# Performance work log

Measured on AMD Instinct MI355X. Metric: run time of the kernel, lower is better.

## Reference

```python
import jax, jax.numpy as jnp
import numpy as np

BLOCK = 8
C = 64


def setup_inputs() -> dict:
    key = jax.random.key(0)
    k = jax.random.split(key, 6)
    B, H, W = 4, 512, 512
    x = jax.random.normal(k[0], (B, C, H, W), jnp.float32)
    # per-channel 8x8 transform matrices (torch.randn init)
    tw = jax.random.normal(k[1], (C, BLOCK, BLOCK), jnp.float32)
    s = 1.0 / np.sqrt(C).astype(np.float32)
    w1 = jax.random.normal(k[2], (C, C), jnp.float32) * s  # 1x1 conv weight [out,in]
    b1 = jax.random.normal(k[3], (C,), jnp.float32) * s
    w2 = jax.random.normal(k[4], (C, C), jnp.float32) * s
    b2 = jax.random.normal(k[5], (C,), jnp.float32) * s
    return {"x": x, "tw": tw, "w1": w1, "b1": b1, "w2": w2, "b2": b2}


def reference(x, tw, w1, b1, w2, b2):
    B, Cc, H, W = x.shape
    bs = BLOCK
    nh, nw = H // bs, W // bs
    # extract 8x8 blocks: [b,c,nh,nw,i,j]
    p = x.reshape(B, Cc, nh, bs, nw, bs).transpose(0, 1, 2, 4, 3, 5)
    # per-channel T @ P @ T^T : out[p,q] = T[p,i] P[i,j] T[q,j]
    t = jnp.einsum('cpi,bcnmij,cqj->bcnmpq', tw, p, tw)
    # fold blocks back to image
    y = t.transpose(0, 1, 2, 4, 3, 5).reshape(B, Cc, H, W)
    # quantization gate: 1x1 conv -> relu -> 1x1 conv -> sigmoid
    g = jnp.einsum('oc,bchw->bohw', w1, y) + b1[None, :, None, None]
    g = jax.nn.relu(g)
    g = jnp.einsum('oc,bchw->bohw', w2, g) + b2[None, :, None, None]
    g = jax.nn.sigmoid(g)
    return y * g
```

## Files before the change

kernel.cpp:

```cpp
#include <hip/hip_runtime.h>

typedef float f4 __attribute__((ext_vector_type(4)));
typedef __attribute__((ext_vector_type(4))) float f32x4;
typedef _Float16 h8 __attribute__((ext_vector_type(8)));

__device__ __forceinline__ void gload_lds16(const float* g, float* l) {
    __builtin_amdgcn_global_load_lds(
        (const __attribute__((address_space(1))) void*)g,
        (__attribute__((address_space(3))) void*)l, 16, 0, 0);
}

__global__ __launch_bounds__(256, 2)
void avif_pipe2(const float* __restrict__ x, const float* __restrict__ twm,
                const float* __restrict__ w1, const float* __restrict__ b1,
                const float* __restrict__ w2, const float* __restrict__ b2,
                float* __restrict__ out)
{
    __shared__ float xs[8192];
    __shared__ ushort ysf[128][64];
    __shared__ ushort hsf[128][64];

    const int t = threadIdx.x;
    const int bid = blockIdx.x;
    const int wc  = bid >> 8;
    const int rem = bid & 255;
    const int hb  = rem & 63;
    const int b   = rem >> 6;

    const int wv = t >> 6, lane = t & 63;
    const int li = lane & 15, lg = lane >> 4, l7 = li & 7;
    const int lb3 = (li >> 3) << 2;

    const float* xslab = x + (((size_t)(b * 64)) * 512 + (size_t)hb * 8) * 512 + wc * 16;
    const float* gp[8];
#pragma unroll
    for (int j = 0; j < 8; ++j) {
        const int G = j * 256 + t;
        const int c = G >> 5;
        const int v = (G & 31) ^ (c & 7);
        const int r = v >> 2, qg = v & 3;
        gp[j] = xslab + (size_t)c * 262144 + r * 512 + qg * 4;
    }
    float* lbase = &xs[wv * 256];

    h8 w1f[2], w2f[2];
    {
        const float* p1 = w1 + (16 * wv + li) * 64 + lg * 8;
        const float* p2 = w2 + (16 * wv + li) * 64 + lg * 8;
#pragma unroll
        for (int kk = 0; kk < 2; ++kk) {
            f4 a = *(const f4*)(p1 + kk * 32);
            f4 d = *(const f4*)(p1 + kk * 32 + 4);
            h8 f;
#pragma unroll
            for (int q = 0; q < 4; ++q) { f[q] = (_Float16)a[q]; f[4 + q] = (_Float16)d[q]; }
            w1f[kk] = f;
            a = *(const f4*)(p2 + kk * 32);
            d = *(const f4*)(p2 + kk * 32 + 4);
#pragma unroll
            for (int q = 0; q < 4; ++q) { f[q] = (_Float16)a[q]; f[4 + q] = (_Float16)d[q]; }
            w2f[kk] = f;
        }
    }
    const int o0 = 16 * wv + 4 * lg;
    const f4 b1v = *(const f4*)(b1 + o0);
    const float b2s = b2[16 * wv + li];
    const int sg0 = ((lg       ^ l7 ^ lb3) << 3);
    const int sg1 = (((4 + lg) ^ l7 ^ lb3) << 3);
    const int go  = o0 >> 3, co = 4 * (lg & 1);
    const int ch  = 16 * wv + li;
    const int cgE = ch >> 3, c7E = li & 7;

    const int pid = t >> 1, h2 = t & 1;
    const int c   = pid & 63, blk = pid >> 6, Q0 = 4 * h2;
    const float* tB = twm + c * 64;
    const int sc = c * 128, swc = c & 7;
    const int cg = c >> 3, c7 = c & 7;

#pragma unroll
    for (int j = 0; j < 8; ++j) gload_lds16(gp[j], lbase + j * 1024);
    asm volatile("s_waitcnt vmcnt(0)" ::: "memory");
    __syncthreads();

    for (int tile = 0; tile < 16; ++tile) {
        const int wt = 2 * tile + wc;

        {
            float M[8][4];
            {
                f4 Ph[8];
#pragma unroll
                for (int i = 0; i < 8; ++i)
                    Ph[i] = *(const f4*)&xs[sc + ((i * 4 + blk * 2) ^ swc) * 4];
#pragma unroll
                for (int qq = 0; qq < 4; ++qq) {
                    f4 Th = *(const f4*)(tB + (Q0 + qq) * 8);
#pragma unroll
                    for (int i = 0; i < 8; ++i) {
                        float s = Ph[i][0] * Th[0];
                        s = fmaf(Ph[i][1], Th[1], s);
                        s = fmaf(Ph[i][2], Th[2], s);
                        s = fmaf(Ph[i][3], Th[3], s);
                        M[i][qq] = s;
                    }
                }
#pragma unroll
                for (int i = 0; i < 8; ++i)
                    Ph[i] = *(const f4*)&xs[sc + ((i * 4 + blk * 2 + 1) ^ swc) * 4];
#pragma unroll
                for (int qq = 0; qq < 4; ++qq) {
                    f4 Th = *(const f4*)(tB + (Q0 + qq) * 8 + 4);
#pragma unroll
                    for (int i = 0; i < 8; ++i) {
                        float s = M[i][qq];
                        s = fmaf(Ph[i][0], Th[0], s);
                        s = fmaf(Ph[i][1], Th[1], s);
                        s = fmaf(Ph[i][2], Th[2], s);
                        s = fmaf(Ph[i][3], Th[3], s);
                        M[i][qq] = s;
                    }
                }
            }
#pragma unroll
            for (int p = 0; p < 8; ++p) {
                f4 a = *(const f4*)(tB + p * 8);
                f4 d = *(const f4*)(tB + p * 8 + 4);
                const int px0 = p * 16 + blk * 8;
#pragma unroll
                for (int qq = 0; qq < 4; ++qq) {
                    const int q = Q0 + qq;
                    float s = a[0] * M[0][qq];
                    s = fmaf(a[1], M[1][qq], s);
                    s = fmaf(a[2], M[2][qq], s);
                    s = fmaf(a[3], M[3][qq], s);
                    s = fmaf(d[0], M[4][qq], s);
                    s = fmaf(d[1], M[5][qq], s);
                    s = fmaf(d[2], M[6][qq], s);
                    s = fmaf(d[3], M[7][qq], s);
                    const int idx = ((cg ^ q ^ (blk << 2)) << 3) | c7;
                    *(_Float16*)&ysf[px0 + q][idx] = (_Float16)s;
                }
            }
        }
        __syncthreads();

        if (tile < 15) {
#pragma unroll
            for (int j = 0; j < 8; ++j)
                gload_lds16(gp[j] + (tile + 1) * 32, lbase + j * 1024);
        }

        f32x4 acc[8];
#pragma unroll
        for (int j = 0; j < 8; ++j) acc[j] = (f32x4){0.f, 0.f, 0.f, 0.f};
#pragma unroll
        for (int j = 0; j < 8; ++j) {
            const int row = 16 * j + li;
            h8 bh0 = *(const h8*)&ysf[row][sg0];
            h8 bh1 = *(const h8*)&ysf[row][sg1];
            acc[j] = __builtin_amdgcn_mfma_f32_16x16x32_f16(w1f[0], bh0, acc[j], 0, 0, 0);
            acc[j] = __builtin_amdgcn_mfma_f32_16x16x32_f16(w1f[1], bh1, acc[j], 0, 0, 0);
        }
#pragma unroll
        for (int j = 0; j < 8; ++j) {
            const int px = 16 * j + li;
            const int idx = ((go ^ l7 ^ lb3) << 3) + co;
            union { _Float16 h[2]; unsigned u; } p01, p23;
            p01.h[0] = (_Float16)fmaxf(acc[j][0] + b1v[0], 0.f);
            p01.h[1] = (_Float16)fmaxf(acc[j][1] + b1v[1], 0.f);
            p23.h[0] = (_Float16)fmaxf(acc[j][2] + b1v[2], 0.f);
            p23.h[1] = (_Float16)fmaxf(acc[j][3] + b1v[3], 0.f);
            *(unsigned*)&hsf[px][idx]     = p01.u;
            *(unsigned*)&hsf[px][idx + 2] = p23.u;
        }
        __syncthreads();

#pragma unroll
        for (int j = 0; j < 8; ++j) acc[j] = (f32x4){0.f, 0.f, 0.f, 0.f};
#pragma unroll
        for (int j = 0; j < 8; ++j) {
            const int row = 16 * j + li;
            h8 ah0 = *(const h8*)&hsf[row][sg0];
            h8 ah1 = *(const h8*)&hsf[row][sg1];
            acc[j] = __builtin_amdgcn_mfma_f32_16x16x32_f16(ah0, w2f[0], acc[j], 0, 0, 0);
            acc[j] = __builtin_amdgcn_mfma_f32_16x16x32_f16(ah1, w2f[1], acc[j], 0, 0, 0);
        }
        float* oB = out + ((size_t)(b * 64) + ch) * 262144
                    + (size_t)(hb * 8) * 512 + wt * 16 + 4 * lg;
#pragma unroll
        for (int j = 0; j < 8; ++j) {
            f4 r;
#pragma unroll
            for (int r4 = 0; r4 < 4; ++r4) {
                const int pc = 4 * lg + r4;
                const int px = 16 * j + pc;
                const int idx = ((cgE ^ (pc & 7) ^ (((pc >> 3) & 1) << 2)) << 3) | c7E;
                float yv = (float)(*(const _Float16*)&ysf[px][idx]);
                float z = acc[j][r4] + b2s;
                float g = __builtin_amdgcn_rcpf(1.f + __expf(-z));
                r[r4] = yv * g;
            }
            *(f4*)(oB + (size_t)j * 512) = r;
        }
        asm volatile("s_waitcnt vmcnt(0)" ::: "memory");
        __syncthreads();
    }
}

extern "C" void kernel_launch(void* const* d_in, const int* in_sizes, int n_in,
                              void* d_out, int out_size, void* d_ws, size_t ws_size,
                              hipStream_t stream) {
    (void)in_sizes; (void)n_in; (void)out_size; (void)d_ws; (void)ws_size;
    const float* x   = (const float*)d_in[0];
    const float* twm = (const float*)d_in[1];
    const float* w1  = (const float*)d_in[2];
    const float* b1  = (const float*)d_in[3];
    const float* w2  = (const float*)d_in[4];
    const float* b2  = (const float*)d_in[5];
    float* out = (float*)d_out;

    avif_pipe2<<<dim3(512), dim3(256), 0, stream>>>(x, twm, w1, b1, w2, b2, out);
}
```

Baseline: 175.2 us.

## Double block size to 512 threads and split per-tile work across eight waves

Raises the workgroup from 256 to 512 threads. Each thread now computes two output columns of the per-channel 8x8 transform instead of four, and the eight waves split the MFMA gate GEMMs by output-channel group and by pixel-row half. The global-to-LDS loads are reissued with half as many loads per thread. The aim is more waves per CU to hide LDS, MFMA and global latency, since the grid gives each CU only about two blocks. The cost is a tighter per-thread register budget under the launch bounds, and each block's barriers now wait on more waves.

```diff
diff --git a/kernel.cpp b/kernel.cpp
--- a/kernel.cpp
+++ b/kernel.cpp
@@ -10,8 +10,8 @@
         (__attribute__((address_space(3))) void*)l, 16, 0, 0);
 }
 
-__global__ __launch_bounds__(256, 2)
-void avif_pipe2(const float* __restrict__ x, const float* __restrict__ twm,
+__global__ __launch_bounds__(512, 2)
+void avif_pipe3(const float* __restrict__ x, const float* __restrict__ twm,
                 const float* __restrict__ w1, const float* __restrict__ b1,
                 const float* __restrict__ w2, const float* __restrict__ b2,
                 float* __restrict__ out)
@@ -30,12 +30,14 @@
     const int wv = t >> 6, lane = t & 63;
     const int li = lane & 15, lg = lane >> 4, l7 = li & 7;
     const int lb3 = (li >> 3) << 2;
+    const int wr = wv & 3;
+    const int wj = wv >> 2;
 
     const float* xslab = x + (((size_t)(b * 64)) * 512 + (size_t)hb * 8) * 512 + wc * 16;
-    const float* gp[8];
-#pragma unroll
-    for (int j = 0; j < 8; ++j) {
-        const int G = j * 256 + t;
+    const float* gp[4];
+#pragma unroll
+    for (int j = 0; j < 4; ++j) {
+        const int G = j * 512 + t;
         const int c = G >> 5;
         const int v = (G & 31) ^ (c & 7);
         const int r = v >> 2, qg = v & 3;
@@ -45,8 +47,8 @@
 
     h8 w1f[2], w2f[2];
     {
-        const float* p1 = w1 + (16 * wv + li) * 64 + lg * 8;
-        const float* p2 = w2 + (16 * wv + li) * 64 + lg * 8;
+        const float* p1 = w1 + (16 * wr + li) * 64 + lg * 8;
+        const float* p2 = w2 + (16 * wr + li) * 64 + lg * 8;
 #pragma unroll
         for (int kk = 0; kk < 2; ++kk) {
             f4 a = *(const f4*)(p1 + kk * 32);
@@ -62,23 +64,25 @@
             w2f[kk] = f;
         }
     }
-    const int o0 = 16 * wv + 4 * lg;
+    const int o0 = 16 * wr + 4 * lg;
     const f4 b1v = *(const f4*)(b1 + o0);
-    const float b2s = b2[16 * wv + li];
+    const float b2s = b2[16 * wr + li];
     const int sg0 = ((lg       ^ l7 ^ lb3) << 3);
     const int sg1 = (((4 + lg) ^ l7 ^ lb3) << 3);
     const int go  = o0 >> 3, co = 4 * (lg & 1);
-    const int ch  = 16 * wv + li;
+    const int ch  = 16 * wr + li;
     const int cgE = ch >> 3, c7E = li & 7;
 
-    const int pid = t >> 1, h2 = t & 1;
-    const int c   = pid & 63, blk = pid >> 6, Q0 = 4 * h2;
+    const int qu  = t & 3;
+    const int pid = t >> 2;
+    const int c   = pid & 63, blk = pid >> 6;
+    const int Q0  = 2 * qu;
     const float* tB = twm + c * 64;
     const int sc = c * 128, swc = c & 7;
     const int cg = c >> 3, c7 = c & 7;
 
 #pragma unroll
-    for (int j = 0; j < 8; ++j) gload_lds16(gp[j], lbase + j * 1024);
+    for (int j = 0; j < 4; ++j) gload_lds16(gp[j], lbase + j * 2048);
     asm volatile("s_waitcnt vmcnt(0)" ::: "memory");
     __syncthreads();
 
@@ -86,14 +90,14 @@
         const int wt = 2 * tile + wc;
 
         {
-            float M[8][4];
+            float M[8][2];
             {
                 f4 Ph[8];
 #pragma unroll
                 for (int i = 0; i < 8; ++i)
                     Ph[i] = *(const f4*)&xs[sc + ((i * 4 + blk * 2) ^ swc) * 4];
 #pragma unroll
-                for (int qq = 0; qq < 4; ++qq) {
+                for (int qq = 0; qq < 2; ++qq) {
                     f4 Th = *(const f4*)(tB + (Q0 + qq) * 8);
 #pragma unroll
                     for (int i = 0; i < 8; ++i) {
@@ -108,7 +112,7 @@
                 for (int i = 0; i < 8; ++i)
                     Ph[i] = *(const f4*)&xs[sc + ((i * 4 + blk * 2 + 1) ^ swc) * 4];
 #pragma unroll
-                for (int qq = 0; qq < 4; ++qq) {
+                for (int qq = 0; qq < 2; ++qq) {
                     f4 Th = *(const f4*)(tB + (Q0 + qq) * 8 + 4);
 #pragma unroll
                     for (int i = 0; i < 8; ++i) {
@@ -127,7 +131,7 @@
                 f4 d = *(const f4*)(tB + p * 8 + 4);
                 const int px0 = p * 16 + blk * 8;
 #pragma unroll
-                for (int qq = 0; qq < 4; ++qq) {
+                for (int qq = 0; qq < 2; ++qq) {
                     const int q = Q0 + qq;
                     float s = a[0] * M[0][qq];
                     s = fmaf(a[1], M[1][qq], s);
@@ -146,49 +150,50 @@
 
         if (tile < 15) {
 #pragma unroll
-            for (int j = 0; j < 8; ++j)
-                gload_lds16(gp[j] + (tile + 1) * 32, lbase + j * 1024);
-        }
-
-        f32x4 acc[8];
-#pragma unroll
-        for (int j = 0; j < 8; ++j) acc[j] = (f32x4){0.f, 0.f, 0.f, 0.f};
-#pragma unroll
-        for (int j = 0; j < 8; ++j) {
-            const int row = 16 * j + li;
+            for (int j = 0; j < 4; ++j)
+                gload_lds16(gp[j] + (tile + 1) * 32, lbase + j * 2048);
+        }
+
+        f32x4 acc[4];
+#pragma unroll
+        for (int jj = 0; jj < 4; ++jj) acc[jj] = (f32x4){0.f, 0.f, 0.f, 0.f};
+#pragma unroll
+        for (int jj = 0; jj < 4; ++jj) {
+            const int row = 16 * (wj * 4 + jj) + li;
             h8 bh0 = *(const h8*)&ysf[row][sg0];
             h8 bh1 = *(const h8*)&ysf[row][sg1];
-            acc[j] = __builtin_amdgcn_mfma_f32_16x16x32_f16(w1f[0], bh0, acc[j], 0, 0, 0);
-            acc[j] = __builtin_amdgcn_mfma_f32_16x16x32_f16(w1f[1], bh1, acc[j], 0, 0, 0);
-        }
-#pragma unroll
-        for (int j = 0; j < 8; ++j) {
-            const int px = 16 * j + li;
+            acc[jj] = __builtin_amdgcn_mfma_f32_16x16x32_f16(w1f[0], bh0, acc[jj], 0, 0, 0);
+            acc[jj] = __builtin_amdgcn_mfma_f32_16x16x32_f16(w1f[1], bh1, acc[jj], 0, 0, 0);
+        }
+#pragma unroll
+        for (int jj = 0; jj < 4; ++jj) {
+            const int px = 16 * (wj * 4 + jj) + li;
             const int idx = ((go ^ l7 ^ lb3) << 3) + co;
             union { _Float16 h[2]; unsigned u; } p01, p23;
-            p01.h[0] = (_Float16)fmaxf(acc[j][0] + b1v[0], 0.f);
-            p01.h[1] = (_Float16)fmaxf(acc[j][1] + b1v[1], 0.f);
-            p23.h[0] = (_Float16)fmaxf(acc[j][2] + b1v[2], 0.f);
-            p23.h[1] = (_Float16)fmaxf(acc[j][3] + b1v[3], 0.f);
+            p01.h[0] = (_Float16)fmaxf(acc[jj][0] + b1v[0], 0.f);
+            p01.h[1] = (_Float16)fmaxf(acc[jj][1] + b1v[1], 0.f);
+            p23.h[0] = (_Float16)fmaxf(acc[jj][2] + b1v[2], 0.f);
+            p23.h[1] = (_Float16)fmaxf(acc[jj][3] + b1v[3], 0.f);
             *(unsigned*)&hsf[px][idx]     = p01.u;
             *(unsigned*)&hsf[px][idx + 2] = p23.u;
         }
         __syncthreads();
 
 #pragma unroll
-        for (int j = 0; j < 8; ++j) acc[j] = (f32x4){0.f, 0.f, 0.f, 0.f};
-#pragma unroll
-        for (int j = 0; j < 8; ++j) {
-            const int row = 16 * j + li;
+        for (int jj = 0; jj < 4; ++jj) acc[jj] = (f32x4){0.f, 0.f, 0.f, 0.f};
+#pragma unroll
+        for (int jj = 0; jj < 4; ++jj) {
+            const int row = 16 * (wj * 4 + jj) + li;
             h8 ah0 = *(const h8*)&hsf[row][sg0];
             h8 ah1 = *(const h8*)&hsf[row][sg1];
-            acc[j] = __builtin_amdgcn_mfma_f32_16x16x32_f16(ah0, w2f[0], acc[j], 0, 0, 0);
-            acc[j] = __builtin_amdgcn_mfma_f32_16x16x32_f16(ah1, w2f[1], acc[j], 0, 0, 0);
+            acc[jj] = __builtin_amdgcn_mfma_f32_16x16x32_f16(ah0, w2f[0], acc[jj], 0, 0, 0);
+            acc[jj] = __builtin_amdgcn_mfma_f32_16x16x32_f16(ah1, w2f[1], acc[jj], 0, 0, 0);
         }
         float* oB = out + ((size_t)(b * 64) + ch) * 262144
                     + (size_t)(hb * 8) * 512 + wt * 16 + 4 * lg;
 #pragma unroll
-        for (int j = 0; j < 8; ++j) {
+        for (int jj = 0; jj < 4; ++jj) {
+            const int j = wj * 4 + jj;
             f4 r;
 #pragma unroll
             for (int r4 = 0; r4 < 4; ++r4) {
@@ -196,7 +201,7 @@
                 const int px = 16 * j + pc;
                 const int idx = ((cgE ^ (pc & 7) ^ (((pc >> 3) & 1) << 2)) << 3) | c7E;
                 float yv = (float)(*(const _Float16*)&ysf[px][idx]);
-                float z = acc[j][r4] + b2s;
+                float z = acc[jj][r4] + b2s;
                 float g = __builtin_amdgcn_rcpf(1.f + __expf(-z));
                 r[r4] = yv * g;
             }
@@ -219,5 +224,5 @@
     const float* b2  = (const float*)d_in[5];
     float* out = (float*)d_out;
 
-    avif_pipe2<<<dim3(512), dim3(256), 0, stream>>>(x, twm, w1, b1, w2, b2, out);
+    avif_pipe3<<<dim3(512), dim3(512), 0, stream>>>(x, twm, w1, b1, w2, b2, out);
 }
```

New measurement: 239.3 us. +36.6%, slower.

## Stage input tiles through registers as fp16 and raise occupancy to three blocks

Applied to the files above, without the earlier changes.

Replaces the direct global-to-LDS async loads with register-staged loads issued at the start of each tile. The data is converted to fp16 and written into a smaller swizzled LDS buffer at the end of the tile. Halving the x staging footprint allows launch bounds of three blocks per CU, and the prefetch overlaps with the transform and MFMA work. The cost is extra registers for staged data, conversion instructions, and fp16 rounding of the input before the 8x8 transform, which lowers precision.

```diff
diff --git a/kernel.cpp b/kernel.cpp
--- a/kernel.cpp
+++ b/kernel.cpp
@@ -3,20 +3,15 @@
 typedef float f4 __attribute__((ext_vector_type(4)));
 typedef __attribute__((ext_vector_type(4))) float f32x4;
 typedef _Float16 h8 __attribute__((ext_vector_type(8)));
-
-__device__ __forceinline__ void gload_lds16(const float* g, float* l) {
-    __builtin_amdgcn_global_load_lds(
-        (const __attribute__((address_space(1))) void*)g,
-        (__attribute__((address_space(3))) void*)l, 16, 0, 0);
-}
-
-__global__ __launch_bounds__(256, 2)
-void avif_pipe2(const float* __restrict__ x, const float* __restrict__ twm,
+typedef _Float16 h4 __attribute__((ext_vector_type(4)));
+
+__global__ __launch_bounds__(256, 3)
+void avif_pipe7(const float* __restrict__ x, const float* __restrict__ twm,
                 const float* __restrict__ w1, const float* __restrict__ b1,
                 const float* __restrict__ w2, const float* __restrict__ b2,
                 float* __restrict__ out)
 {
-    __shared__ float xs[8192];
+    __shared__ ushort xs[64 * 128];
     __shared__ ushort ysf[128][64];
     __shared__ ushort hsf[128][64];
 
@@ -32,16 +27,16 @@
     const int lb3 = (li >> 3) << 2;
 
     const float* xslab = x + (((size_t)(b * 64)) * 512 + (size_t)hb * 8) * 512 + wc * 16;
-    const float* gp[8];
-#pragma unroll
-    for (int j = 0; j < 8; ++j) {
-        const int G = j * 256 + t;
-        const int c = G >> 5;
-        const int v = (G & 31) ^ (c & 7);
-        const int r = v >> 2, qg = v & 3;
-        gp[j] = xslab + (size_t)c * 262144 + r * 512 + qg * 4;
+    const float* gq[4];
+    int ls[4];
+#pragma unroll
+    for (int j = 0; j < 4; ++j) {
+        const int vid = j * 256 + t;
+        const int cc = vid >> 4, sub = vid & 15;
+        const int r = sub >> 1, half = sub & 1;
+        gq[j] = xslab + (size_t)cc * 262144 + r * 512 + half * 8;
+        ls[j] = cc * 128 + ((sub ^ (cc & 15)) << 3);
     }
-    float* lbase = &xs[wv * 256];
 
     h8 w1f[2], w2f[2];
     {
@@ -74,24 +69,48 @@
     const int pid = t >> 1, h2 = t & 1;
     const int c   = pid & 63, blk = pid >> 6, Q0 = 4 * h2;
     const float* tB = twm + c * 64;
-    const int sc = c * 128, swc = c & 7;
+    const int xc = c * 128, c15 = c & 15;
     const int cg = c >> 3, c7 = c & 7;
 
-#pragma unroll
-    for (int j = 0; j < 8; ++j) gload_lds16(gp[j], lbase + j * 1024);
-    asm volatile("s_waitcnt vmcnt(0)" ::: "memory");
+    f4 Sa[4], Sd[4];
+    auto stage_load = [&](int tile) {
+#pragma unroll
+        for (int j = 0; j < 4; ++j) {
+            Sa[j] = *(const f4*)(gq[j] + tile * 32);
+            Sd[j] = *(const f4*)(gq[j] + tile * 32 + 4);
+        }
+    };
+    auto stage_write = [&]() {
+#pragma unroll
+        for (int j = 0; j < 4; ++j) {
+            h8 hv;
+#pragma unroll
+            for (int e = 0; e < 4; ++e) {
+                hv[e]     = (_Float16)Sa[j][e];
+                hv[4 + e] = (_Float16)Sd[j][e];
+            }
+            *(h8*)&xs[ls[j]] = hv;
+        }
+    };
+
+    stage_load(0);
+    stage_write();
     __syncthreads();
 
     for (int tile = 0; tile < 16; ++tile) {
         const int wt = 2 * tile + wc;
+        if (tile < 15) stage_load(tile + 1);
 
         {
             float M[8][4];
             {
                 f4 Ph[8];
 #pragma unroll
-                for (int i = 0; i < 8; ++i)
-                    Ph[i] = *(const f4*)&xs[sc + ((i * 4 + blk * 2) ^ swc) * 4];
+                for (int i = 0; i < 8; ++i) {
+                    h4 hv = *(const h4*)&xs[xc + (((i * 2 + blk) ^ c15) << 3)];
+#pragma unroll
+                    for (int e = 0; e < 4; ++e) Ph[i][e] = (float)hv[e];
+                }
 #pragma unroll
                 for (int qq = 0; qq < 4; ++qq) {
                     f4 Th = *(const f4*)(tB + (Q0 + qq) * 8);
@@ -105,8 +124,11 @@
                     }
                 }
 #pragma unroll
-                for (int i = 0; i < 8; ++i)
-                    Ph[i] = *(const f4*)&xs[sc + ((i * 4 + blk * 2 + 1) ^ swc) * 4];
+                for (int i = 0; i < 8; ++i) {
+                    h4 hv = *(const h4*)&xs[xc + (((i * 2 + blk) ^ c15) << 3) + 4];
+#pragma unroll
+                    for (int e = 0; e < 4; ++e) Ph[i][e] = (float)hv[e];
+                }
 #pragma unroll
                 for (int qq = 0; qq < 4; ++qq) {
                     f4 Th = *(const f4*)(tB + (Q0 + qq) * 8 + 4);
@@ -144,12 +166,6 @@
         }
         __syncthreads();
 
-        if (tile < 15) {
-#pragma unroll
-            for (int j = 0; j < 8; ++j)
-                gload_lds16(gp[j] + (tile + 1) * 32, lbase + j * 1024);
-        }
-
         f32x4 acc[8];
 #pragma unroll
         for (int j = 0; j < 8; ++j) acc[j] = (f32x4){0.f, 0.f, 0.f, 0.f};
@@ -202,7 +218,7 @@
             }
             *(f4*)(oB + (size_t)j * 512) = r;
         }
-        asm volatile("s_waitcnt vmcnt(0)" ::: "memory");
+        if (tile < 15) stage_write();
         __syncthreads();
     }
 }
@@ -219,5 +235,5 @@
     const float* b2  = (const float*)d_in[5];
     float* out = (float*)d_out;
 
-    avif_pipe2<<<dim3(512), dim3(256), 0, stream>>>(x, twm, w1, b1, w2, b2, out);
+    avif_pipe7<<<dim3(512), dim3(256), 0, stream>>>(x, twm, w1, b1, w2, b2, out);
 }
```

Result: slower. 300.7 us (+71.6%).
